# Kernel optimization log

Measured on AMD Instinct MI355X. Metric: run time of the kernel, lower is better.

The kernel has to match this reference:

```python
import jax, jax.numpy as jnp
import numpy as np

BATCH, SEQ, IN, HID, CLS = 512, 1024, 64, 256, 10

def setup_inputs() -> dict:
    key = jax.random.key(0)
    k1, k2, k3, k4, k5 = jax.random.split(key, 5)
    s_ih = 1.0 / np.sqrt(IN + HID)
    s_ho = 1.0 / np.sqrt(HID)
    return {
        "inputs": jax.random.normal(k1, (BATCH, SEQ, IN), dtype=jnp.float32),
        "W_ih": jax.random.normal(k2, (IN + HID, HID), dtype=jnp.float32) * s_ih,
        "b_ih": jax.random.normal(k3, (HID,), dtype=jnp.float32) * s_ih,
        "W_ho": jax.random.normal(k4, (HID, CLS), dtype=jnp.float32) * s_ho,
        "b_ho": jax.random.normal(k5, (CLS,), dtype=jnp.float32) * s_ho,
    }

def reference(inputs, W_ih, b_ih, W_ho, b_ho):
    # Elman RNN: hidden_{t} = tanh([x_t, hidden_{t-1}] @ W_ih + b_ih)
    B, S, I = inputs.shape
    H = W_ih.shape[1]
    # split W_ih into input and hidden blocks (equivalent to concat+matmul)
    Wx = W_ih[:I]      # (I, H)
    Wh = W_ih[I:]      # (H, H)
    h0 = jnp.zeros((B, H), dtype=inputs.dtype)
    # precompute input projections for all timesteps at once: (B, S, H)
    xproj = jnp.einsum('bsi,ih->bsh', inputs, Wx) + b_ih

    def step(h, xp_t):
        h_new = jnp.tanh(xp_t + h @ Wh)
        return h_new, None

    h_final, _ = jax.lax.scan(step, h0, jnp.swapaxes(xproj, 0, 1))  # scan over time
    return h_final @ W_ho + b_ho  # (B, CLS)
```

## Files before the change

kernel.cpp:

```cpp
#include <hip/hip_runtime.h>
#include <hip/hip_bf16.h>


#define BATCH 512
#define SEQ   1024
#define INP   64
#define HID   256
#define CLS   10
#define NTHREADS 512
#define TSCALE 2.8853900817779268f

typedef short bf16x8 __attribute__((ext_vector_type(8)));
typedef float f32x4  __attribute__((ext_vector_type(4)));

static __device__ __forceinline__ unsigned short f2bf(float f) {
  __hip_bfloat16 h = __float2bfloat16(f);
  return *reinterpret_cast<unsigned short*>(&h);
}
static __device__ __forceinline__ float bf2f(unsigned short b) {
  union { unsigned int u; float f; } v; v.u = ((unsigned int)b) << 16;
  return v.f;
}
static __device__ __forceinline__ unsigned int cvt_pk_bf16(float lo, float hi) {
  unsigned int r;
  asm("v_cvt_pk_bf16_f32 %0, %1, %2" : "=v"(r) : "v"(lo), "v"(hi));
  return r;
}
static __device__ __forceinline__ float fast_exp2(float x) {
#if __has_builtin(__builtin_amdgcn_exp2f)
  return __builtin_amdgcn_exp2f(x);
#else
  return __exp2f(x);
#endif
}
static __device__ __forceinline__ float fast_rcp(float x) {
#if __has_builtin(__builtin_amdgcn_rcpf)
  return __builtin_amdgcn_rcpf(x);
#else
  return 1.0f / x;
#endif
}
static __device__ __forceinline__ float tanh_scaled(float s) {
  return 1.0f - 2.0f * fast_rcp(1.0f + fast_exp2(s));
}

#define MFMA16(A, B, C) __builtin_amdgcn_mfma_f32_16x16x32_bf16(A, B, C, 0, 0, 0)

#define BARRIER() asm volatile("s_waitcnt lgkmcnt(0)\n\ts_barrier" ::: "memory")

#define STEP(T, CUR, XR) do {                                                   \
        \
    if (wave == 0) {                                                            \
      ((unsigned int*)sX[(CUR) ^ 1])[lane] = cvt_pk_bf16(XR.x, XR.y);           \
      int tn_ = (T) + 3; tn_ = tn_ < SEQ ? tn_ : SEQ - 1;                       \
      XR = *(const float2*)&xstage[(size_t)tn_ * INP];                          \
    }                                                                           \
    f32x4 acc0 = {bias0, bias0, bias0, bias0};                                  \
    f32x4 acc1 = {bias1, bias1, bias1, bias1};                                  \
                         \
    if (frow < 2) {                                                             \
      aP0 = *(const bf16x8*)&sX[CUR][frow][g8];                                 \
      aP1 = *(const bf16x8*)&sX[CUR][frow][32 + g8];                            \
      aQ0 = *(const bf16x8*)&sH[CUR][frow][0 * 32 + g8];                        \
      aQ1 = *(const bf16x8*)&sH[CUR][frow][1 * 32 + g8];                        \
    }                                                                           \
    acc0 = MFMA16(aP0, bw[0][0], acc0); acc1 = MFMA16(aP0, bw[0][1], acc1);     \
    acc0 = MFMA16(aP1, bw[1][0], acc0); acc1 = MFMA16(aP1, bw[1][1], acc1);     \
    __builtin_amdgcn_sched_barrier(0);                                          \
    if (frow < 2) {                                                             \
      aP0 = *(const bf16x8*)&sH[CUR][frow][2 * 32 + g8];                        \
      aP1 = *(const bf16x8*)&sH[CUR][frow][3 * 32 + g8];                        \
    }                                                                           \
    acc0 = MFMA16(aQ0, bw[2][0], acc0); acc1 = MFMA16(aQ0, bw[2][1], acc1);     \
    acc0 = MFMA16(aQ1, bw[3][0], acc0); acc1 = MFMA16(aQ1, bw[3][1], acc1);     \
    __builtin_amdgcn_sched_barrier(0);                                          \
    if (frow < 2) {                                                             \
      aQ0 = *(const bf16x8*)&sH[CUR][frow][4 * 32 + g8];                        \
      aQ1 = *(const bf16x8*)&sH[CUR][frow][5 * 32 + g8];                        \
    }                                                                           \
    acc0 = MFMA16(aP0, bw[4][0], acc0); acc1 = MFMA16(aP0, bw[4][1], acc1);     \
    acc0 = MFMA16(aP1, bw[5][0], acc0); acc1 = MFMA16(aP1, bw[5][1], acc1);     \
    __builtin_amdgcn_sched_barrier(0);                                          \
    if (frow < 2) {                                                             \
      aP0 = *(const bf16x8*)&sH[CUR][frow][6 * 32 + g8];                        \
      aP1 = *(const bf16x8*)&sH[CUR][frow][7 * 32 + g8];                        \
    }                                                                           \
    acc0 = MFMA16(aQ0, bw[6][0], acc0); acc1 = MFMA16(aQ0, bw[6][1], acc1);     \
    acc0 = MFMA16(aQ1, bw[7][0], acc0); acc1 = MFMA16(aQ1, bw[7][1], acc1);     \
    __builtin_amdgcn_sched_barrier(0);                                          \
    acc0 = MFMA16(aP0, bw[8][0], acc0); acc1 = MFMA16(aP0, bw[8][1], acc1);     \
    acc0 = MFMA16(aP1, bw[9][0], acc0); acc1 = MFMA16(aP1, bw[9][1], acc1);     \
            \
    float t00 = tanh_scaled(acc0[0]);                   \
    float t10 = tanh_scaled(acc1[0]);                   \
    float t01 = tanh_scaled(acc0[1]);                   \
    float t11 = tanh_scaled(acc1[1]);                   \
    if (g == 0) {                                                               \
      unsigned int* hd_ = (unsigned int*)sH[(CUR) ^ 1];                         \
      hd_[0 * 128 + 16 * wave + frow] = cvt_pk_bf16(t00, t10);                  \
      hd_[1 * 128 + 16 * wave + frow] = cvt_pk_bf16(t01, t11);                  \
    }                                                                           \
    BARRIER();                                                                  \
  } while (0)

__global__ __launch_bounds__(NTHREADS, 2)
void rnn_scan_kernel(const float* __restrict__ x,
                     const float* __restrict__ W_ih,
                     const float* __restrict__ b_ih,
                     const float* __restrict__ W_ho,
                     const float* __restrict__ b_ho,
                     float* __restrict__ out) {
  __shared__ __align__(16) unsigned short sH[2][2][HID];
  __shared__ __align__(16) unsigned short sX[2][2][INP];

  const int tid  = threadIdx.x;
  const int lane = tid & 63;
  const int wave = tid >> 6;
  const int b0   = blockIdx.x * 2;

  const int g    = (lane >> 4) & 3;
  const int g8   = g * 8;
  const int frow = lane & 15;

  bf16x8 bw[10][2];
  const int colE = 32 * wave + 2 * frow;
  const float bias0 = b_ih[colE] * TSCALE;
  const float bias1 = b_ih[colE + 1] * TSCALE;
#pragma unroll
  for (int q = 0; q < 2; ++q) {
#pragma unroll
    for (int kt = 0; kt < 10; ++kt) {
      bf16x8 v;
#pragma unroll
      for (int i = 0; i < 8; ++i)
        v[i] = (short)f2bf(W_ih[(size_t)(kt * 32 + g * 8 + i) * HID + colE + q] * TSCALE);
      bw[kt][q] = v;
    }
  }

  const int xrow = lane >> 5, xcp = lane & 31;
  const float* xstage = x + (size_t)(b0 + xrow) * SEQ * INP + xcp * 2;
  float2 xrA = make_float2(0.f, 0.f), xrB = make_float2(0.f, 0.f);

  bf16x8 aP0 = {}, aP1 = {}, aQ0 = {}, aQ1 = {};

  if (tid < 256) ((unsigned int*)sH[0])[tid] = 0u;
  if (wave == 0) {
    float2 v0 = *(const float2*)&xstage[0];
    ((unsigned int*)sX[0])[lane] = cvt_pk_bf16(v0.x, v0.y);
    xrA = *(const float2*)&xstage[(size_t)1 * INP];
    xrB = *(const float2*)&xstage[(size_t)2 * INP];
  }
  BARRIER();

#pragma unroll 1
  for (int t = 0; t < SEQ; t += 2) {
    STEP(t,     0, xrA);
    STEP(t + 1, 1, xrB);
  }

  if (tid < 2 * CLS) {
    const int r = tid / CLS, cl = tid - r * CLS;
    float s = b_ho[cl];
#pragma unroll 8
    for (int k = 0; k < HID; ++k)
      s += bf2f(sH[0][r][k]) * W_ho[(size_t)k * CLS + cl];
    out[(size_t)(b0 + r) * CLS + cl] = s;
  }
}

extern "C" void kernel_launch(void* const* d_in, const int* in_sizes, int n_in,
                              void* d_out, int out_size, void* d_ws, size_t ws_size,
                              hipStream_t stream) {
  const float* x    = (const float*)d_in[0];
  const float* W_ih = (const float*)d_in[1];
  const float* b_ih = (const float*)d_in[2];
  const float* W_ho = (const float*)d_in[3];
  const float* b_ho = (const float*)d_in[4];
  float* out = (float*)d_out;

  rnn_scan_kernel<<<BATCH / 2, NTHREADS, 0, stream>>>(x, W_ih, b_ih, W_ho, b_ho, out);
}
```

Before: 547.7 us.

## Split MFMA accumulator chains, retile shared state by k-tile, raise MFMA priority

Each step's single dependent chain of 10 MFMAs per output is split into two interleaved accumulator chains (a/b), which are summed before tanh. This shortens the serial MFMA dependency latency on the recurrent critical path. Shared hidden and input buffers are re-laid out as [ktile][row][32] so the per-row fragment reads and the hidden writes use a tile-major layout. s_setprio is raised around the MFMA section to favour this wave's issue.

```diff
diff --git a/kernel.cpp b/kernel.cpp
--- a/kernel.cpp
+++ b/kernel.cpp
@@ -51,54 +51,59 @@
 #define STEP(T, CUR, XR) do {                                                   \
         \
     if (wave == 0) {                                                            \
-      ((unsigned int*)sX[(CUR) ^ 1])[lane] = cvt_pk_bf16(XR.x, XR.y);           \
+      ((unsigned int*)sX[(CUR) ^ 1])[(xcp >> 4) * 32 + xrow * 16 + (xcp & 15)]  \
+          = cvt_pk_bf16(XR.x, XR.y);                                            \
       int tn_ = (T) + 3; tn_ = tn_ < SEQ ? tn_ : SEQ - 1;                       \
       XR = *(const float2*)&xstage[(size_t)tn_ * INP];                          \
     }                                                                           \
-    f32x4 acc0 = {bias0, bias0, bias0, bias0};                                  \
-    f32x4 acc1 = {bias1, bias1, bias1, bias1};                                  \
+    f32x4 acc0a = {bias0, bias0, bias0, bias0};                                 \
+    f32x4 acc1a = {bias1, bias1, bias1, bias1};                                 \
+    f32x4 acc0b = {0.f, 0.f, 0.f, 0.f};                                         \
+    f32x4 acc1b = {0.f, 0.f, 0.f, 0.f};                                         \
                          \
     if (frow < 2) {                                                             \
-      aP0 = *(const bf16x8*)&sX[CUR][frow][g8];                                 \
-      aP1 = *(const bf16x8*)&sX[CUR][frow][32 + g8];                            \
-      aQ0 = *(const bf16x8*)&sH[CUR][frow][0 * 32 + g8];                        \
-      aQ1 = *(const bf16x8*)&sH[CUR][frow][1 * 32 + g8];                        \
+      aP0 = *(const bf16x8*)&sX[CUR][0][frow][g8];                              \
+      aP1 = *(const bf16x8*)&sX[CUR][1][frow][g8];                              \
+      aQ0 = *(const bf16x8*)&sH[CUR][0][frow][g8];                              \
+      aQ1 = *(const bf16x8*)&sH[CUR][1][frow][g8];                              \
     }                                                                           \
-    acc0 = MFMA16(aP0, bw[0][0], acc0); acc1 = MFMA16(aP0, bw[0][1], acc1);     \
-    acc0 = MFMA16(aP1, bw[1][0], acc0); acc1 = MFMA16(aP1, bw[1][1], acc1);     \
+    __builtin_amdgcn_s_setprio(1);                                              \
+    acc0a = MFMA16(aP0, bw[0][0], acc0a); acc1a = MFMA16(aP0, bw[0][1], acc1a); \
+    acc0b = MFMA16(aP1, bw[1][0], acc0b); acc1b = MFMA16(aP1, bw[1][1], acc1b); \
     __builtin_amdgcn_sched_barrier(0);                                          \
     if (frow < 2) {                                                             \
-      aP0 = *(const bf16x8*)&sH[CUR][frow][2 * 32 + g8];                        \
-      aP1 = *(const bf16x8*)&sH[CUR][frow][3 * 32 + g8];                        \
+      aP0 = *(const bf16x8*)&sH[CUR][2][frow][g8];                              \
+      aP1 = *(const bf16x8*)&sH[CUR][3][frow][g8];                              \
     }                                                                           \
-    acc0 = MFMA16(aQ0, bw[2][0], acc0); acc1 = MFMA16(aQ0, bw[2][1], acc1);     \
-    acc0 = MFMA16(aQ1, bw[3][0], acc0); acc1 = MFMA16(aQ1, bw[3][1], acc1);     \
+    acc0a = MFMA16(aQ0, bw[2][0], acc0a); acc1a = MFMA16(aQ0, bw[2][1], acc1a); \
+    acc0b = MFMA16(aQ1, bw[3][0], acc0b); acc1b = MFMA16(aQ1, bw[3][1], acc1b); \
     __builtin_amdgcn_sched_barrier(0);                                          \
     if (frow < 2) {                                                             \
-      aQ0 = *(const bf16x8*)&sH[CUR][frow][4 * 32 + g8];                        \
-      aQ1 = *(const bf16x8*)&sH[CUR][frow][5 * 32 + g8];                        \
+      aQ0 = *(const bf16x8*)&sH[CUR][4][frow][g8];                              \
+      aQ1 = *(const bf16x8*)&sH[CUR][5][frow][g8];                              \
     }                                                                           \
-    acc0 = MFMA16(aP0, bw[4][0], acc0); acc1 = MFMA16(aP0, bw[4][1], acc1);     \
-    acc0 = MFMA16(aP1, bw[5][0], acc0); acc1 = MFMA16(aP1, bw[5][1], acc1);     \
+    acc0a = MFMA16(aP0, bw[4][0], acc0a); acc1a = MFMA16(aP0, bw[4][1], acc1a); \
+    acc0b = MFMA16(aP1, bw[5][0], acc0b); acc1b = MFMA16(aP1, bw[5][1], acc1b); \
     __builtin_amdgcn_sched_barrier(0);                                          \
     if (frow < 2) {                                                             \
-      aP0 = *(const bf16x8*)&sH[CUR][frow][6 * 32 + g8];                        \
-      aP1 = *(const bf16x8*)&sH[CUR][frow][7 * 32 + g8];                        \
+      aP0 = *(const bf16x8*)&sH[CUR][6][frow][g8];                              \
+      aP1 = *(const bf16x8*)&sH[CUR][7][frow][g8];                              \
     }                                                                           \
-    acc0 = MFMA16(aQ0, bw[6][0], acc0); acc1 = MFMA16(aQ0, bw[6][1], acc1);     \
-    acc0 = MFMA16(aQ1, bw[7][0], acc0); acc1 = MFMA16(aQ1, bw[7][1], acc1);     \
+    acc0a = MFMA16(aQ0, bw[6][0], acc0a); acc1a = MFMA16(aQ0, bw[6][1], acc1a); \
+    acc0b = MFMA16(aQ1, bw[7][0], acc0b); acc1b = MFMA16(aQ1, bw[7][1], acc1b); \
     __builtin_amdgcn_sched_barrier(0);                                          \
-    acc0 = MFMA16(aP0, bw[8][0], acc0); acc1 = MFMA16(aP0, bw[8][1], acc1);     \
-    acc0 = MFMA16(aP1, bw[9][0], acc0); acc1 = MFMA16(aP1, bw[9][1], acc1);     \
+    acc0a = MFMA16(aP0, bw[8][0], acc0a); acc1a = MFMA16(aP0, bw[8][1], acc1a); \
+    acc0b = MFMA16(aP1, bw[9][0], acc0b); acc1b = MFMA16(aP1, bw[9][1], acc1b); \
+    __builtin_amdgcn_s_setprio(0);                                              \
             \
-    float t00 = tanh_scaled(acc0[0]);                   \
-    float t10 = tanh_scaled(acc1[0]);                   \
-    float t01 = tanh_scaled(acc0[1]);                   \
-    float t11 = tanh_scaled(acc1[1]);                   \
+    float t00 = tanh_scaled(acc0a[0] + acc0b[0]);       \
+    float t10 = tanh_scaled(acc1a[0] + acc1b[0]);       \
+    float t01 = tanh_scaled(acc0a[1] + acc0b[1]);       \
+    float t11 = tanh_scaled(acc1a[1] + acc1b[1]);       \
     if (g == 0) {                                                               \
       unsigned int* hd_ = (unsigned int*)sH[(CUR) ^ 1];                         \
-      hd_[0 * 128 + 16 * wave + frow] = cvt_pk_bf16(t00, t10);                  \
-      hd_[1 * 128 + 16 * wave + frow] = cvt_pk_bf16(t01, t11);                  \
+      hd_[wave * 32 + frow]      = cvt_pk_bf16(t00, t10);            \
+      hd_[wave * 32 + 16 + frow] = cvt_pk_bf16(t01, t11);            \
     }                                                                           \
     BARRIER();                                                                  \
   } while (0)
@@ -110,8 +115,8 @@
                      const float* __restrict__ W_ho,
                      const float* __restrict__ b_ho,
                      float* __restrict__ out) {
-  __shared__ __align__(16) unsigned short sH[2][2][HID];
-  __shared__ __align__(16) unsigned short sX[2][2][INP];
+  __shared__ __align__(16) unsigned short sH[2][8][2][32];
+  __shared__ __align__(16) unsigned short sX[2][2][2][32];
 
   const int tid  = threadIdx.x;
   const int lane = tid & 63;
@@ -147,7 +152,8 @@
   if (tid < 256) ((unsigned int*)sH[0])[tid] = 0u;
   if (wave == 0) {
     float2 v0 = *(const float2*)&xstage[0];
-    ((unsigned int*)sX[0])[lane] = cvt_pk_bf16(v0.x, v0.y);
+    ((unsigned int*)sX[0])[(xcp >> 4) * 32 + xrow * 16 + (xcp & 15)]
+        = cvt_pk_bf16(v0.x, v0.y);
     xrA = *(const float2*)&xstage[(size_t)1 * INP];
     xrB = *(const float2*)&xstage[(size_t)2 * INP];
   }
@@ -164,7 +170,7 @@
     float s = b_ho[cl];
 #pragma unroll 8
     for (int k = 0; k < HID; ++k)
-      s += bf2f(sH[0][r][k]) * W_ho[(size_t)k * CLS + cl];
+      s += bf2f(sH[0][k >> 5][r][k & 31]) * W_ho[(size_t)k * CLS + cl];
     out[(size_t)(b0 + r) * CLS + cl] = s;
   }
 }
```

Result: faster. 529.3 us (-3.4%).
